# Performance work log

Measured on AMD Instinct MI355X. Metric: run time of the kernel, lower is better.

## Reference

```python
import jax, jax.numpy as jnp
import numpy as np

B, T = 32, 128
D, H, HD = 512, 8, 64
FF, E, N = 2048, 8, 3
NF = 16            # Fourier features
VOCAB, FEAT = 119, 200
SCALE = 10.0
EPS = 1e-5


def layernorm(x, g, b):
    m = jnp.mean(x, axis=-1, keepdims=True)
    v = jnp.mean((x - m) ** 2, axis=-1, keepdims=True)
    return (x - m) * jax.lax.rsqrt(v + EPS) * g + b


def setup_inputs() -> dict:
    key = jax.random.key(0)
    ks = jax.random.split(key, 32)
    f32 = jnp.float32
    inp = {
        "src": jax.random.randint(ks[0], (B, T), 0, VOCAB),
        "frac": jax.random.uniform(ks[1], (B, T), dtype=f32),
        "embed_table": jax.random.normal(ks[2], (VOCAB, FEAT), f32),
        "W_m2v": jax.random.normal(ks[3], (FEAT, D), f32) * 0.05,
        "b_m2v": jnp.zeros((D,), f32),
        "pb_W": jax.random.normal(ks[4], (1, NF), f32) * 0.1,
        "pb_b": jax.random.uniform(ks[5], (NF,), f32) * 2 * np.pi,
        "pb_a": jax.random.normal(ks[6], (NF,), f32),
        "Wk": jax.random.normal(ks[7], (N, D, D), f32) * 0.03,
        "bk": jnp.zeros((N, D), f32),
        "Wv": jax.random.normal(ks[8], (N, D, D), f32) * 0.03,
        "bv": jnp.zeros((N, D), f32),
        "Wo": jax.random.normal(ks[9], (N, D, D), f32) * 0.03,
        "bo": jnp.zeros((N, D), f32),
        "ln1_g": jnp.ones((N, D), f32),
        "ln1_b": jnp.zeros((N, D), f32),
        "ln2_g": jnp.ones((N, D), f32),
        "ln2_b": jnp.zeros((N, D), f32),
        "gate_W": jax.random.normal(ks[10], (N, D, E), f32) * 0.05,
        "gate_b": jnp.zeros((N, E), f32),
        "eW1": jax.random.normal(ks[11], (N, E, D, FF), f32) * 0.03,
        "eb1": jnp.zeros((N, E, FF), f32),
        "eW2": jax.random.normal(ks[12], (N, E, FF, D), f32) * 0.02,
        "eb2": jnp.zeros((N, E, D), f32),
    }
    return inp


def reference(src, frac, embed_table, W_m2v, b_m2v, pb_W, pb_b, pb_a,
              Wk, bk, Wv, bv, Wo, bo, ln1_g, ln1_b, ln2_g, ln2_b,
              gate_W, gate_b, eW1, eb1, eW2, eb2):
    # Embedder: mat2vec lookup + linear projection
    x = embed_table[src] @ W_m2v + b_m2v                      # [B,T,D]

    # Fourier positional bias: pb[b,i,j] = cos((frac_j - frac_i)*scale * W + b) @ a
    diffs = (frac[:, None, :] - frac[:, :, None]) * SCALE     # [B,T,T]
    rff = jnp.cos(diffs[..., None] * pb_W[0] + pb_b)          # [B,T,T,NF]
    pb = rff @ pb_a                                           # [B,T,T]

    for i in range(N):
        # --- Fourier-bias attention ---
        K = (x @ Wk[i] + bk[i]).reshape(B, T, H, HD).transpose(0, 2, 1, 3)  # [B,H,T,HD]
        V = (x @ Wv[i] + bv[i]).reshape(B, T, H, HD).transpose(0, 2, 1, 3)
        # scores[b,h,i,j,d] = K[b,h,j,d] + pb[b,i,j]; weighted = sum_j scores*V
        # factor: sum_j K*V (indep of i) + sum_j pb[b,i,j]*V[b,h,j,d]
        kv = jnp.sum(K * V, axis=2)                           # [B,H,HD]
        pbv = jnp.einsum('bij,bhjd->bhid', pb, V)             # [B,H,T,HD]
        wv = (pbv + kv[:, :, None, :]).transpose(0, 2, 1, 3).reshape(B, T, D)
        x = layernorm(x + wv @ Wo[i] + bo[i], ln1_g[i], ln1_b[i])

        # --- MoE FFN, top-2 gating (eval mode: no dropout/noise) ---
        probs = jax.nn.softmax(x @ gate_W[i] + gate_b[i], axis=-1)   # [B,T,E]
        top2_s, top2_e = jax.lax.top_k(probs, 2)                     # [B,T,2]
        w = jnp.sum(jax.nn.one_hot(top2_e, E, dtype=x.dtype) * top2_s[..., None], axis=2)  # [B,T,E]
        h = jax.nn.relu(jnp.einsum('btd,edf->btef', x, eW1[i]) + eb1[i])  # [B,T,E,FF]
        eo = jnp.einsum('btef,efd->bted', h, eW2[i]) + eb2[i]             # [B,T,E,D]
        ff = jnp.einsum('bte,bted->btd', w, eo)
        x = layernorm(x + ff, ln2_g[i], ln2_b[i])
    return x
```

## Files before the change

### kernel.cpp

```cpp
#include <hip/hip_runtime.h>
#include <math.h>

#define B_    32
#define T_    128
#define D_    512
#define FF_   2048
#define E_    8
#define NL_   3
#define NF_   16
#define FEAT_ 200
#define BT_   4096

#define GB_   64
#define TPB_  (BT_ / GB_)

typedef short bf16x8 __attribute__((ext_vector_type(8)));
typedef float f32x4  __attribute__((ext_vector_type(4)));

__device__ inline unsigned short f2bf(float f) {
    unsigned u = __float_as_uint(f);
    unsigned r = (u + 0x7fffu + ((u >> 16) & 1u)) >> 16;
    return (unsigned short)r;
}
__device__ inline void split_bf(float f, unsigned short& h, unsigned short& l) {
    h = f2bf(f);
    float fh = __uint_as_float(((unsigned)h) << 16);
    l = f2bf(f - fh);
}

__device__ __forceinline__ void ld_g2l(const unsigned short* g, unsigned short* l)
{
    __builtin_amdgcn_global_load_lds(
        (const __attribute__((address_space(1))) unsigned int*)(uintptr_t)g,
        (__attribute__((address_space(3))) unsigned int*)(uintptr_t)l,
        16, 0, 0);
}

template <int MODE, bool SPLITOUT, bool RELU>
__global__ __launch_bounds__(256)
void mgemm_k(const unsigned short* __restrict__ Ah, const unsigned short* __restrict__ Al,
             const unsigned short* __restrict__ Bh, const unsigned short* __restrict__ Bl,
             const float* __restrict__ bias,
             float* __restrict__ Cf, unsigned short* __restrict__ Ch,
             unsigned short* __restrict__ Cl,
             int M, int K, int N, long strB, int strBias,
             const int* __restrict__ counts, const int* __restrict__ offsets,
             const int* __restrict__ tok_list)
{
    const int z  = blockIdx.z;
    const int m0 = blockIdx.y * 64, n0 = blockIdx.x * 128;
    int rows, rowoff = 0;
    if constexpr (MODE != 0) {
        rows = counts[z];
        if (m0 >= rows) return;
        rowoff = offsets[z];
    } else {
        rows = M;
    }
    const unsigned short* Bhb = Bh + (long)z * strB;
    const unsigned short* Blb = Bl + (long)z * strB;
    const float* biasb = bias + (long)z * strBias;

    __shared__ unsigned short S[2][12288];

    const int tid  = threadIdx.x;
    const int w    = tid >> 6, lane = tid & 63;
    const int wm = w & 1, wn = w >> 1;
    const int l15 = lane & 15, quad = lane >> 4;

    const int arow  = w * 16 + (lane >> 2);
    const int brow0 = w * 32 + (lane >> 2);
    const int brow1 = brow0 + 16;
    const int sseg  = (lane & 3) ^ ((lane >> 3) & 3);
    const int laA   = w * 512;
    const int lbB0  = w * 1024;
    const int lbB1  = w * 1024 + 512;

    long gaA;
    if constexpr (MODE == 1) {
        int m_a = m0 + arow; if (m_a >= rows) m_a = rows - 1;
        gaA = tok_list[z * BT_ + m_a];
    } else if constexpr (MODE == 2) {
        int m_a = m0 + arow; if (m_a >= rows) m_a = rows - 1;
        gaA = (long)rowoff + m_a;
    } else {
        gaA = m0 + arow;
    }
    const long aoff  = gaA * (long)K + sseg * 8;
    const long boff0 = (long)(n0 + brow0) * K + sseg * 8;
    const long boff1 = (long)(n0 + brow1) * K + sseg * 8;

    f32x4 acc[2][4];
#pragma unroll
    for (int i = 0; i < 2; ++i)
#pragma unroll
        for (int j = 0; j < 4; ++j) acc[i][j] = (f32x4)0.f;

    const int xq = quad ^ ((l15 >> 1) & 3);

    {
        unsigned short* Sb = S[0];
        ld_g2l(Ah  + aoff,  Sb + 0    + laA);
        ld_g2l(Al  + aoff,  Sb + 2048 + laA);
        ld_g2l(Bhb + boff0, Sb + 4096 + lbB0);
        ld_g2l(Bhb + boff1, Sb + 4096 + lbB1);
        ld_g2l(Blb + boff0, Sb + 8192 + lbB0);
        ld_g2l(Blb + boff1, Sb + 8192 + lbB1);
    }

    unsigned short* Scur = S[0];
    unsigned short* Snxt = S[1];

    for (int k0 = 0; k0 < K; k0 += 32) {
        __syncthreads();

        if (k0 + 32 < K) {
            int kn = k0 + 32;
            ld_g2l(Ah  + aoff  + kn, Snxt + 0    + laA);
            ld_g2l(Al  + aoff  + kn, Snxt + 2048 + laA);
            ld_g2l(Bhb + boff0 + kn, Snxt + 4096 + lbB0);
            ld_g2l(Bhb + boff1 + kn, Snxt + 4096 + lbB1);
            ld_g2l(Blb + boff0 + kn, Snxt + 8192 + lbB0);
            ld_g2l(Blb + boff1 + kn, Snxt + 8192 + lbB1);
        }

        bf16x8 ah2[2], al2[2], bh4[4], bl4[4];
#pragma unroll
        for (int i = 0; i < 2; ++i) {
            int ro = (wm * 32 + i * 16 + l15) * 32 + xq * 8;
            ah2[i] = *(const bf16x8*)&Scur[0    + ro];
            al2[i] = *(const bf16x8*)&Scur[2048 + ro];
        }
#pragma unroll
        for (int j = 0; j < 4; ++j) {
            int ro = (wn * 64 + j * 16 + l15) * 32 + xq * 8;
            bh4[j] = *(const bf16x8*)&Scur[4096 + ro];
            bl4[j] = *(const bf16x8*)&Scur[8192 + ro];
        }
#pragma unroll
        for (int i = 0; i < 2; ++i)
#pragma unroll
            for (int j = 0; j < 4; ++j) {
                acc[i][j] = __builtin_amdgcn_mfma_f32_16x16x32_bf16(al2[i], bh4[j], acc[i][j], 0, 0, 0);
                acc[i][j] = __builtin_amdgcn_mfma_f32_16x16x32_bf16(ah2[i], bl4[j], acc[i][j], 0, 0, 0);
                acc[i][j] = __builtin_amdgcn_mfma_f32_16x16x32_bf16(ah2[i], bh4[j], acc[i][j], 0, 0, 0);
            }

        unsigned short* t = Scur; Scur = Snxt; Snxt = t;
    }

#pragma unroll
    for (int i = 0; i < 2; ++i) {
#pragma unroll
        for (int r = 0; r < 4; ++r) {
            int gm = m0 + wm * 32 + i * 16 + quad * 4 + r;
            if (MODE != 0 && gm >= rows) continue;
            long crow = (MODE != 0) ? ((long)rowoff + gm) : (long)gm;
#pragma unroll
            for (int j = 0; j < 4; ++j) {
                int col = n0 + wn * 64 + j * 16 + l15;
                float v = acc[i][j][r] + biasb[col];
                if constexpr (RELU) v = fmaxf(v, 0.f);
                if constexpr (SPLITOUT) {
                    unsigned short h, l;
                    split_bf(v, h, l);
                    Ch[crow * (long)N + col] = h;
                    Cl[crow * (long)N + col] = l;
                } else {
                    Cf[crow * (long)N + col] = v;
                }
            }
        }
    }
}

template <bool WF32, bool SPLIT>
__global__ __launch_bounds__(256)
void gemm_k(const float* __restrict__ A, const float* __restrict__ Bm,
            const float* __restrict__ bias, float* __restrict__ C,
            unsigned short* __restrict__ Oh, unsigned short* __restrict__ Ol,
            int K, int lda, int ldb, int ldc,
            long strA, long strB, long strC, int strBias)
{
    const int z  = blockIdx.z;
    const int m0 = blockIdx.y * 64, n0 = blockIdx.x * 64;
    const float* Ab    = A    + (long)z * strA;
    const float* Bb    = Bm   + (long)z * strB;
    const float* biasb = bias + (long)z * strBias;

    __shared__ float As[16][68];
    __shared__ float Bs[16][64];

    const int tid = threadIdx.x;
    const int tx  = tid & 15, ty = tid >> 4;
    const int ar  = tid >> 2;
    const int akc = (tid & 3) * 4;
    const float* Arow = Ab + (long)(m0 + ar) * lda;
    const int bkr = tid >> 4;
    const int bnc = (tid & 15) * 4;

    float acc[4][4];
#pragma unroll
    for (int i = 0; i < 4; ++i)
#pragma unroll
        for (int j = 0; j < 4; ++j) acc[i][j] = 0.f;

    for (int k0 = 0; k0 < K; k0 += 16) {
        if (k0 + 16 <= K) {
            float4 a = *(const float4*)(Arow + k0 + akc);
            As[akc + 0][ar] = a.x; As[akc + 1][ar] = a.y;
            As[akc + 2][ar] = a.z; As[akc + 3][ar] = a.w;
        } else {
#pragma unroll
            for (int j = 0; j < 4; ++j) {
                int kk = k0 + akc + j;
                As[akc + j][ar] = (kk < K) ? Arow[kk] : 0.f;
            }
        }
        {
            int kk = k0 + bkr;
            float4 b;
            if (kk < K) b = *(const float4*)(Bb + (long)kk * ldb + n0 + bnc);
            else        b = make_float4(0.f, 0.f, 0.f, 0.f);
            *(float4*)&Bs[bkr][bnc] = b;
        }
        __syncthreads();
#pragma unroll
        for (int k = 0; k < 16; ++k) {
            float4 av = *(const float4*)&As[k][ty * 4];
            float4 bv = *(const float4*)&Bs[k][tx * 4];
            float am[4] = {av.x, av.y, av.z, av.w};
            float bn[4] = {bv.x, bv.y, bv.z, bv.w};
#pragma unroll
            for (int i = 0; i < 4; ++i)
#pragma unroll
                for (int j = 0; j < 4; ++j)
                    acc[i][j] = fmaf(am[i], bn[j], acc[i][j]);
        }
        __syncthreads();
    }
#pragma unroll
    for (int i = 0; i < 4; ++i) {
        long base = ((long)z * strC) + (long)(m0 + ty * 4 + i) * ldc + n0 + tx * 4;
        const float* bp = biasb + n0 + tx * 4;
#pragma unroll
        for (int j = 0; j < 4; ++j) {
            float v = acc[i][j] + bp[j];
            if constexpr (WF32) C[base + j] = v;
            if constexpr (SPLIT) {
                unsigned short h, l;
                split_bf(v, h, l);
                Oh[base + j] = h;
                Ol[base + j] = l;
            }
        }
    }
}

__global__ __launch_bounds__(256)
void transpose_split_k(const float* __restrict__ in,
                       unsigned short* __restrict__ oh, unsigned short* __restrict__ ol,
                       int R, int C, long strIn, long strOut)
{
    __shared__ float tile[32][33];
    const float* I = in + (long)blockIdx.z * strIn;
    unsigned short* OH = oh + (long)blockIdx.z * strOut;
    unsigned short* OL = ol + (long)blockIdx.z * strOut;
    int c0 = blockIdx.x * 32, r0 = blockIdx.y * 32;
    int tx = threadIdx.x & 31, ty = threadIdx.x >> 5;
#pragma unroll
    for (int i = 0; i < 4; ++i)
        tile[ty + i * 8][tx] = I[(long)(r0 + ty + i * 8) * C + c0 + tx];
    __syncthreads();
#pragma unroll
    for (int i = 0; i < 4; ++i) {
        unsigned short h, l;
        split_bf(tile[tx][ty + i * 8], h, l);
        long o = (long)(c0 + ty + i * 8) * R + r0 + tx;
        OH[o] = h; OL[o] = l;
    }
}

__global__ void bias_cat_k(const float* __restrict__ a, const float* __restrict__ b,
                           float* __restrict__ o)
{
    int i = blockIdx.x * 256 + threadIdx.x;
    o[i] = (i < D_) ? a[i] : b[i - D_];
}

__global__ void embed_gather_k(const int* __restrict__ src,
                               const float* __restrict__ table,
                               float* __restrict__ emb)
{
    int t = blockIdx.x;
    int v = src[t];
    for (int k = threadIdx.x; k < FEAT_; k += 256)
        emb[t * FEAT_ + k] = table[v * FEAT_ + k];
}

__global__ __launch_bounds__(256)
void pb_k(const float* __restrict__ frac, const float* __restrict__ pbW,
          const float* __restrict__ pbb, const float* __restrict__ pba,
          float* __restrict__ pb)
{
    int idx = blockIdx.x * 256 + threadIdx.x;
    int b = idx >> 14;
    int i = (idx >> 7) & 127;
    int j = idx & 127;
    float diff = (frac[b * T_ + j] - frac[b * T_ + i]) * 10.0f;
    float s = 0.f;
#pragma unroll
    for (int f = 0; f < NF_; ++f)
        s = fmaf(cosf(fmaf(diff, pbW[f], pbb[f])), pba[f], s);
    pb[idx] = s;
}

__global__ __launch_bounds__(256)
void kv_k(const float* __restrict__ KV, float* __restrict__ kv)
{
    int idx = blockIdx.x * 256 + threadIdx.x;
    int b = idx >> 9, c = idx & 511;
    const float* Kp = KV + (long)b * T_ * 1024 + c;
    float s = 0.f;
    for (int t = 0; t < T_; ++t) {
        const float* p = Kp + t * 1024;
        s = fmaf(p[0], p[D_], s);
    }
    kv[idx] = s;
}

__global__ __launch_bounds__(256)
void ln_res_k(const float* __restrict__ x, const float* __restrict__ add,
              const float* __restrict__ g, const float* __restrict__ b,
              float* __restrict__ out, unsigned short* __restrict__ oh,
              unsigned short* __restrict__ ol)
{
    int wave = threadIdx.x >> 6, lane = threadIdx.x & 63;
    int row = blockIdx.x * 4 + wave;
    const float* xr = x   + (long)row * D_ + lane * 8;
    const float* ar = add + (long)row * D_ + lane * 8;
    float v[8]; float s = 0.f;
#pragma unroll
    for (int j = 0; j < 8; ++j) { v[j] = xr[j] + ar[j]; s += v[j]; }
#pragma unroll
    for (int off = 32; off > 0; off >>= 1) s += __shfl_xor(s, off, 64);
    float mean = s * (1.f / D_);
    float q = 0.f;
#pragma unroll
    for (int j = 0; j < 8; ++j) { float d = v[j] - mean; q += d * d; }
#pragma unroll
    for (int off = 32; off > 0; off >>= 1) q += __shfl_xor(q, off, 64);
    float inv = rsqrtf(q * (1.f / D_) + 1e-5f);
    float* orow = out + (long)row * D_ + lane * 8;
    unsigned short* hrow = oh + (long)row * D_ + lane * 8;
    unsigned short* lrow = ol + (long)row * D_ + lane * 8;
#pragma unroll
    for (int j = 0; j < 8; ++j) {
        int c = lane * 8 + j;
        float o = (v[j] - mean) * inv * g[c] + b[c];
        orow[j] = o;
        unsigned short hh, ll;
        split_bf(o, hh, ll);
        hrow[j] = hh; lrow[j] = ll;
    }
}

__global__ __launch_bounds__(256)
void ln_moe_k(const float* __restrict__ x, const float* __restrict__ eo,
              const int* __restrict__ tok_slot, const float* __restrict__ tok_w,
              const int* __restrict__ offsets,
              const float* __restrict__ g, const float* __restrict__ b,
              float* __restrict__ out, unsigned short* __restrict__ oh,
              unsigned short* __restrict__ ol)
{
    int wave = threadIdx.x >> 6, lane = threadIdx.x & 63;
    int row = blockIdx.x * 4 + wave;
    int  c0 = tok_slot[row * 2], c1 = tok_slot[row * 2 + 1];
    float w0 = tok_w[row * 2],  w1 = tok_w[row * 2 + 1];
    long r0 = offsets[c0 >> 12] + (c0 & 4095);
    long r1 = offsets[c1 >> 12] + (c1 & 4095);
    const float* xr = x  + (long)row * D_ + lane * 8;
    const float* e0 = eo + r0 * D_ + lane * 8;
    const float* e1 = eo + r1 * D_ + lane * 8;
    float v[8]; float s = 0.f;
#pragma unroll
    for (int j = 0; j < 8; ++j) {
        v[j] = xr[j] + w0 * e0[j] + w1 * e1[j];
        s += v[j];
    }
#pragma unroll
    for (int off = 32; off > 0; off >>= 1) s += __shfl_xor(s, off, 64);
    float mean = s * (1.f / D_);
    float q = 0.f;
#pragma unroll
    for (int j = 0; j < 8; ++j) { float d = v[j] - mean; q += d * d; }
#pragma unroll
    for (int off = 32; off > 0; off >>= 1) q += __shfl_xor(q, off, 64);
    float inv = rsqrtf(q * (1.f / D_) + 1e-5f);
    float* orow = out + (long)row * D_ + lane * 8;
    unsigned short* hrow = oh + (long)row * D_ + lane * 8;
    unsigned short* lrow = ol + (long)row * D_ + lane * 8;
#pragma unroll
    for (int j = 0; j < 8; ++j) {
        int c = lane * 8 + j;
        float o = (v[j] - mean) * inv * g[c] + b[c];
        orow[j] = o;
        unsigned short hh, ll;
        split_bf(o, hh, ll);
        hrow[j] = hh; lrow[j] = ll;
    }
}

__global__ __launch_bounds__(256)
void gate_k(const float* __restrict__ x, const float* __restrict__ gW,
            const float* __restrict__ gb, int* __restrict__ counts,
            int* __restrict__ tok_list, int* __restrict__ tok_slot,
            float* __restrict__ tok_w)
{
    __shared__ int scnt[E_];
    __shared__ int sbase[E_];
    __shared__ int sent[TPB_][2];

    const int wave = threadIdx.x >> 6, lane = threadIdx.x & 63;
    const int e  = lane & 7;
    const int ch = lane >> 3;
    const int t0 = blockIdx.x * TPB_;

    if (threadIdx.x < E_) scnt[threadIdx.x] = 0;
    __syncthreads();

    for (int it = 0; it < TPB_ / 4; ++it) {
        const int tl = it * 4 + wave;
        const int t  = t0 + tl;

        const float4* x4 = (const float4*)(x + (long)t * D_ + ch * 64);
        const float*  wr = gW + (long)ch * 64 * E_ + e;
        float acc = 0.f;
#pragma unroll
        for (int d4 = 0; d4 < 16; ++d4) {
            float4 xv = x4[d4];
            acc = fmaf(xv.x, wr[(d4 * 4 + 0) * 8], acc);
            acc = fmaf(xv.y, wr[(d4 * 4 + 1) * 8], acc);
            acc = fmaf(xv.z, wr[(d4 * 4 + 2) * 8], acc);
            acc = fmaf(xv.w, wr[(d4 * 4 + 3) * 8], acc);
        }
        acc += __shfl_xor(acc, 8, 64);
        acc += __shfl_xor(acc, 16, 64);
        acc += __shfl_xor(acc, 32, 64);
        acc += gb[e];

        float lg[8];
#pragma unroll
        for (int ee = 0; ee < 8; ++ee)
            lg[ee] = __shfl(acc, (lane & 56) | ee, 64);

        float m = lg[0];
#pragma unroll
        for (int ee = 1; ee < 8; ++ee) m = fmaxf(m, lg[ee]);
        float p[8]; float s = 0.f;
#pragma unroll
        for (int ee = 0; ee < 8; ++ee) { p[ee] = expf(lg[ee] - m); s += p[ee]; }
        float inv = 1.f / s;
        int e1 = 0;
#pragma unroll
        for (int ee = 1; ee < 8; ++ee) if (p[ee] > p[e1]) e1 = ee;
        int e2 = (e1 == 0) ? 1 : 0;
#pragma unroll
        for (int ee = 0; ee < 8; ++ee) {
            if (ee == e1) continue;
            if (p[ee] > p[e2]) e2 = ee;
        }

        if (lane == 0) {
            int ls1 = atomicAdd(&scnt[e1], 1);
            int ls2 = atomicAdd(&scnt[e2], 1);
            sent[tl][0] = (e1 << 12) | ls1;
            sent[tl][1] = (e2 << 12) | ls2;
            tok_w[t * 2]     = p[e1] * inv;
            tok_w[t * 2 + 1] = p[e2] * inv;
        }
    }
    __syncthreads();

    if (threadIdx.x < E_)
        sbase[threadIdx.x] = atomicAdd(&counts[threadIdx.x], scnt[threadIdx.x]);
    __syncthreads();

    for (int tl = threadIdx.x; tl < TPB_; tl += 256) {
        const int t = t0 + tl;
#pragma unroll
        for (int kk = 0; kk < 2; ++kk) {
            int v    = sent[tl][kk];
            int ee   = v >> 12;
            int slot = sbase[ee] + (v & 4095);
            tok_list[ee * BT_ + slot] = t;
            tok_slot[t * 2 + kk] = (ee << 12) | slot;
        }
    }
}

__global__ void zero_counts_k(int* __restrict__ counts)
{
    if (threadIdx.x < E_) counts[threadIdx.x] = 0;
}

__global__ void scan_k(const int* __restrict__ counts, int* __restrict__ offsets)
{
    if (threadIdx.x == 0) {
        int s = 0;
        for (int e = 0; e < E_; ++e) { offsets[e] = s; s += counts[e]; }
    }
}

extern "C" void kernel_launch(void* const* d_in, const int* in_sizes, int n_in,
                              void* d_out, int out_size, void* d_ws, size_t ws_size,
                              hipStream_t stream)
{
    const int*   src   = (const int*)  d_in[0];
    const float* frac  = (const float*)d_in[1];
    const float* table = (const float*)d_in[2];
    const float* W_m2v = (const float*)d_in[3];
    const float* b_m2v = (const float*)d_in[4];
    const float* pbW   = (const float*)d_in[5];
    const float* pbb   = (const float*)d_in[6];
    const float* pba   = (const float*)d_in[7];
    const float* Wk    = (const float*)d_in[8];
    const float* bk    = (const float*)d_in[9];
    const float* Wv    = (const float*)d_in[10];
    const float* bv    = (const float*)d_in[11];
    const float* Wo    = (const float*)d_in[12];
    const float* bo    = (const float*)d_in[13];
    const float* ln1g  = (const float*)d_in[14];
    const float* ln1b  = (const float*)d_in[15];
    const float* ln2g  = (const float*)d_in[16];
    const float* ln2b  = (const float*)d_in[17];
    const float* gW    = (const float*)d_in[18];
    const float* gb    = (const float*)d_in[19];
    const float* eW1   = (const float*)d_in[20];
    const float* eb1   = (const float*)d_in[21];
    const float* eW2   = (const float*)d_in[22];
    const float* eb2   = (const float*)d_in[23];

    float* ws   = (float*)d_ws;
    float* x    = ws;  ws += (long)BT_ * D_;
    float* pb   = ws;  ws += (long)B_ * T_ * T_;
    float* eo   = ws;  ws += (long)2 * BT_ * D_;
    float* kv   = ws;  ws += B_ * D_;
    float* tokw = ws;  ws += 2 * BT_;
    float* kvbias = ws; ws += 2 * D_;
    unsigned short* us = (unsigned short*)ws;
    unsigned short* x_h   = us;  us += (long)BT_ * D_;
    unsigned short* x_l   = us;  us += (long)BT_ * D_;
    unsigned short* Wkv_h = us;  us += (long)2 * D_ * D_;
    unsigned short* Wkv_l = us;  us += (long)2 * D_ * D_;
    unsigned short* Wo_h  = us;  us += (long)D_ * D_;
    unsigned short* Wo_l  = us;  us += (long)D_ * D_;
    unsigned short* e1_h  = us;  us += (long)E_ * FF_ * D_;
    unsigned short* e1_l  = us;  us += (long)E_ * FF_ * D_;
    unsigned short* e2_h  = us;  us += (long)E_ * D_ * FF_;
    unsigned short* e2_l  = us;  us += (long)E_ * D_ * FF_;
    int* counts  = (int*)us;
    int* offsets = counts + 8;
    int* toklist = offsets + 8;
    int* tokslot = toklist + E_ * BT_;
    char* ar = (char*)(tokslot + 2 * BT_);
    ar = (char*)(((size_t)ar + 255) & ~(size_t)255);
    unsigned short* h_h = (unsigned short*)ar;
    unsigned short* h_l = h_h + (long)2 * BT_ * FF_;
    float* emb  = (float*)ar;
    float* KVb  = emb + (long)BT_ * FEAT_;
    float* tmp  = KVb + (long)BT_ * 2 * D_;
    unsigned short* wv_h = (unsigned short*)(tmp + (long)BT_ * D_);
    unsigned short* wv_l = wv_h + (long)BT_ * D_;

    embed_gather_k<<<BT_, 256, 0, stream>>>(src, table, emb);
    gemm_k<true, true><<<dim3(8, 64, 1), 256, 0, stream>>>(
        emb, W_m2v, b_m2v, x, x_h, x_l, FEAT_, FEAT_, D_, D_, 0, 0, 0, 0);

    pb_k<<<(B_ * T_ * T_) / 256, 256, 0, stream>>>(frac, pbW, pbb, pba, pb);

    for (int i = 0; i < NL_; ++i) {
        transpose_split_k<<<dim3(16, 16, 1), 256, 0, stream>>>(
            Wk + (long)i * D_ * D_, Wkv_h, Wkv_l, D_, D_, 0, 0);
        transpose_split_k<<<dim3(16, 16, 1), 256, 0, stream>>>(
            Wv + (long)i * D_ * D_, Wkv_h + (long)D_ * D_, Wkv_l + (long)D_ * D_,
            D_, D_, 0, 0);
        transpose_split_k<<<dim3(16, 16, 1), 256, 0, stream>>>(
            Wo + (long)i * D_ * D_, Wo_h, Wo_l, D_, D_, 0, 0);
        transpose_split_k<<<dim3(64, 16, E_), 256, 0, stream>>>(
            eW1 + (long)i * E_ * D_ * FF_, e1_h, e1_l, D_, FF_,
            (long)D_ * FF_, (long)FF_ * D_);
        transpose_split_k<<<dim3(16, 64, E_), 256, 0, stream>>>(
            eW2 + (long)i * E_ * FF_ * D_, e2_h, e2_l, FF_, D_,
            (long)FF_ * D_, (long)D_ * FF_);
        bias_cat_k<<<4, 256, 0, stream>>>(bk + i * D_, bv + i * D_, kvbias);

        mgemm_k<0, false, false><<<dim3(8, 64, 1), 256, 0, stream>>>(
            x_h, x_l, Wkv_h, Wkv_l, kvbias,
            KVb, nullptr, nullptr, BT_, D_, 2 * D_, 0, 0,
            nullptr, nullptr, nullptr);

        kv_k<<<(B_ * D_) / 256, 256, 0, stream>>>(KVb, kv);

        gemm_k<false, true><<<dim3(8, 2, B_), 256, 0, stream>>>(
            pb, KVb + D_, kv, nullptr, wv_h, wv_l, T_, T_, 2 * D_, D_,
            (long)T_ * T_, (long)T_ * 2 * D_, (long)T_ * D_, D_);

        mgemm_k<0, false, false><<<dim3(4, 64, 1), 256, 0, stream>>>(
            wv_h, wv_l, Wo_h, Wo_l, bo + i * D_,
            tmp, nullptr, nullptr, BT_, D_, D_, 0, 0, nullptr, nullptr, nullptr);

        ln_res_k<<<BT_ / 4, 256, 0, stream>>>(x, tmp, ln1g + i * D_, ln1b + i * D_,
                                              x, x_h, x_l);

        zero_counts_k<<<1, 64, 0, stream>>>(counts);
        gate_k<<<GB_, 256, 0, stream>>>(x, gW + (long)i * D_ * E_, gb + i * E_,
                                        counts, toklist, tokslot, tokw);
        scan_k<<<1, 1, 0, stream>>>(counts, offsets);

        mgemm_k<1, true, true><<<dim3(16, 64, E_), 256, 0, stream>>>(
            x_h, x_l, e1_h, e1_l, eb1 + (long)i * E_ * FF_,
            nullptr, h_h, h_l, 0, D_, FF_,
            (long)FF_ * D_, FF_, counts, offsets, toklist);
        mgemm_k<2, false, false><<<dim3(4, 64, E_), 256, 0, stream>>>(
            h_h, h_l, e2_h, e2_l, eb2 + (long)i * E_ * D_,
            eo, nullptr, nullptr, 0, FF_, D_,
            (long)D_ * FF_, D_, counts, offsets, toklist);

        float* dst = (i == NL_ - 1) ? (float*)d_out : x;
        ln_moe_k<<<BT_ / 4, 256, 0, stream>>>(x, eo, tokslot, tokw, offsets,
                                              ln2g + i * D_, ln2b + i * D_,
                                              dst, x_h, x_l);
    }
}
```

Baseline: 1.226 ms.

## Enlarge split-bf16 MFMA GEMM tile to 128x128 with 512-thread blocks

```diff
diff --git a/kernel.cpp b/kernel.cpp
--- a/kernel.cpp
+++ b/kernel.cpp
@@ -37,7 +37,7 @@
 }
 
 template <int MODE, bool SPLITOUT, bool RELU>
-__global__ __launch_bounds__(256)
+__global__ __launch_bounds__(512)
 void mgemm_k(const unsigned short* __restrict__ Ah, const unsigned short* __restrict__ Al,
              const unsigned short* __restrict__ Bh, const unsigned short* __restrict__ Bl,
              const float* __restrict__ bias,
@@ -48,7 +48,7 @@
              const int* __restrict__ tok_list)
 {
     const int z  = blockIdx.z;
-    const int m0 = blockIdx.y * 64, n0 = blockIdx.x * 128;
+    const int m0 = blockIdx.y * 128, n0 = blockIdx.x * 128;
     int rows, rowoff = 0;
     if constexpr (MODE != 0) {
         rows = counts[z];
@@ -61,34 +61,29 @@
     const unsigned short* Blb = Bl + (long)z * strB;
     const float* biasb = bias + (long)z * strBias;
 
-    __shared__ unsigned short S[2][12288];
+    __shared__ unsigned short S[2][4 * 4096];
 
     const int tid  = threadIdx.x;
     const int w    = tid >> 6, lane = tid & 63;
-    const int wm = w & 1, wn = w >> 1;
+    const int wm = w & 3, wn = w >> 2;
     const int l15 = lane & 15, quad = lane >> 4;
 
-    const int arow  = w * 16 + (lane >> 2);
-    const int brow0 = w * 32 + (lane >> 2);
-    const int brow1 = brow0 + 16;
-    const int sseg  = (lane & 3) ^ ((lane >> 3) & 3);
-    const int laA   = w * 512;
-    const int lbB0  = w * 1024;
-    const int lbB1  = w * 1024 + 512;
+    const int srow = tid >> 2;
+    const int sseg = (tid & 3) ^ ((tid >> 3) & 3);
+    const int lbW  = w * 512;
 
     long gaA;
     if constexpr (MODE == 1) {
-        int m_a = m0 + arow; if (m_a >= rows) m_a = rows - 1;
+        int m_a = m0 + srow; if (m_a >= rows) m_a = rows - 1;
         gaA = tok_list[z * BT_ + m_a];
     } else if constexpr (MODE == 2) {
-        int m_a = m0 + arow; if (m_a >= rows) m_a = rows - 1;
+        int m_a = m0 + srow; if (m_a >= rows) m_a = rows - 1;
         gaA = (long)rowoff + m_a;
     } else {
-        gaA = m0 + arow;
-    }
-    const long aoff  = gaA * (long)K + sseg * 8;
-    const long boff0 = (long)(n0 + brow0) * K + sseg * 8;
-    const long boff1 = (long)(n0 + brow1) * K + sseg * 8;
+        gaA = m0 + srow;
+    }
+    const long aoff = gaA * (long)K + sseg * 8;
+    const long boff = (long)(n0 + srow) * K + sseg * 8;
 
     f32x4 acc[2][4];
 #pragma unroll
@@ -100,12 +95,10 @@
 
     {
         unsigned short* Sb = S[0];
-        ld_g2l(Ah  + aoff,  Sb + 0    + laA);
-        ld_g2l(Al  + aoff,  Sb + 2048 + laA);
-        ld_g2l(Bhb + boff0, Sb + 4096 + lbB0);
-        ld_g2l(Bhb + boff1, Sb + 4096 + lbB1);
-        ld_g2l(Blb + boff0, Sb + 8192 + lbB0);
-        ld_g2l(Blb + boff1, Sb + 8192 + lbB1);
+        ld_g2l(Ah  + aoff, Sb + 0 * 4096 + lbW);
+        ld_g2l(Al  + aoff, Sb + 1 * 4096 + lbW);
+        ld_g2l(Bhb + boff, Sb + 2 * 4096 + lbW);
+        ld_g2l(Blb + boff, Sb + 3 * 4096 + lbW);
     }
 
     unsigned short* Scur = S[0];
@@ -116,26 +109,24 @@
 
         if (k0 + 32 < K) {
             int kn = k0 + 32;
-            ld_g2l(Ah  + aoff  + kn, Snxt + 0    + laA);
-            ld_g2l(Al  + aoff  + kn, Snxt + 2048 + laA);
-            ld_g2l(Bhb + boff0 + kn, Snxt + 4096 + lbB0);
-            ld_g2l(Bhb + boff1 + kn, Snxt + 4096 + lbB1);
-            ld_g2l(Blb + boff0 + kn, Snxt + 8192 + lbB0);
-            ld_g2l(Blb + boff1 + kn, Snxt + 8192 + lbB1);
+            ld_g2l(Ah  + aoff + kn, Snxt + 0 * 4096 + lbW);
+            ld_g2l(Al  + aoff + kn, Snxt + 1 * 4096 + lbW);
+            ld_g2l(Bhb + boff + kn, Snxt + 2 * 4096 + lbW);
+            ld_g2l(Blb + boff + kn, Snxt + 3 * 4096 + lbW);
         }
 
         bf16x8 ah2[2], al2[2], bh4[4], bl4[4];
 #pragma unroll
         for (int i = 0; i < 2; ++i) {
             int ro = (wm * 32 + i * 16 + l15) * 32 + xq * 8;
-            ah2[i] = *(const bf16x8*)&Scur[0    + ro];
-            al2[i] = *(const bf16x8*)&Scur[2048 + ro];
+            ah2[i] = *(const bf16x8*)&Scur[0 * 4096 + ro];
+            al2[i] = *(const bf16x8*)&Scur[1 * 4096 + ro];
         }
 #pragma unroll
         for (int j = 0; j < 4; ++j) {
             int ro = (wn * 64 + j * 16 + l15) * 32 + xq * 8;
-            bh4[j] = *(const bf16x8*)&Scur[4096 + ro];
-            bl4[j] = *(const bf16x8*)&Scur[8192 + ro];
+            bh4[j] = *(const bf16x8*)&Scur[2 * 4096 + ro];
+            bl4[j] = *(const bf16x8*)&Scur[3 * 4096 + ro];
         }
 #pragma unroll
         for (int i = 0; i < 2; ++i)
@@ -595,7 +586,7 @@
             (long)FF_ * D_, (long)D_ * FF_);
         bias_cat_k<<<4, 256, 0, stream>>>(bk + i * D_, bv + i * D_, kvbias);
 
-        mgemm_k<0, false, false><<<dim3(8, 64, 1), 256, 0, stream>>>(
+        mgemm_k<0, false, false><<<dim3(8, 32, 1), 512, 0, stream>>>(
             x_h, x_l, Wkv_h, Wkv_l, kvbias,
             KVb, nullptr, nullptr, BT_, D_, 2 * D_, 0, 0,
             nullptr, nullptr, nullptr);
@@ -606,7 +597,7 @@
             pb, KVb + D_, kv, nullptr, wv_h, wv_l, T_, T_, 2 * D_, D_,
             (long)T_ * T_, (long)T_ * 2 * D_, (long)T_ * D_, D_);
 
-        mgemm_k<0, false, false><<<dim3(4, 64, 1), 256, 0, stream>>>(
+        mgemm_k<0, false, false><<<dim3(4, 32, 1), 512, 0, stream>>>(
             wv_h, wv_l, Wo_h, Wo_l, bo + i * D_,
             tmp, nullptr, nullptr, BT_, D_, D_, 0, 0, nullptr, nullptr, nullptr);
 
@@ -618,11 +609,11 @@
                                         counts, toklist, tokslot, tokw);
         scan_k<<<1, 1, 0, stream>>>(counts, offsets);
 
-        mgemm_k<1, true, true><<<dim3(16, 64, E_), 256, 0, stream>>>(
+        mgemm_k<1, true, true><<<dim3(16, 32, E_), 512, 0, stream>>>(
             x_h, x_l, e1_h, e1_l, eb1 + (long)i * E_ * FF_,
             nullptr, h_h, h_l, 0, D_, FF_,
             (long)FF_ * D_, FF_, counts, offsets, toklist);
-        mgemm_k<2, false, false><<<dim3(4, 64, E_), 256, 0, stream>>>(
+        mgemm_k<2, false, false><<<dim3(4, 32, E_), 512, 0, stream>>>(
             h_h, h_l, e2_h, e2_l, eb2 + (long)i * E_ * D_,
             eo, nullptr, nullptr, 0, FF_, D_,
             (long)D_ * FF_, D_, counts, offsets, toklist);
```

Result: faster. 1.183 ms (-3.5%).
